# Optimization experiments

Measured on AMD Instinct MI355X. Metric: run time of the kernel, lower is better.

Reference implementation:

```python
import jax, jax.numpy as jnp
import numpy as np

H, W = 48, 48
L = H * W            # 2304 tokens
D = 256              # d_model
NH = 8               # heads (self and memory attn)
FF = 1024            # dim_feedforward
T = 2                # memory frames
BS = 1
GN_GROUPS = 32       # GNActDWConv2d default groups


def layernorm(x, g, b, eps=1e-5):
    m = jnp.mean(x, -1, keepdims=True)
    v = jnp.mean((x - m) ** 2, -1, keepdims=True)
    return (x - m) * jax.lax.rsqrt(v + eps) * g + b


def linear(x, Wt, b):
    # torch nn.Linear convention: Wt is [out, in]
    return x @ Wt.T + b


def mha_core(Q, K, V, nhead):
    # Q [Lq, bs, C], K/V [Lk, bs, C]; AOT MultiheadAttention core (eval: no dropout)
    Lq, bs, C = Q.shape
    hd = C // nhead
    Qh = (Q / np.float32(np.sqrt(hd))).reshape(Lq, bs, nhead, hd).transpose(1, 2, 0, 3)
    Kh = K.reshape(-1, bs, nhead, hd).transpose(1, 2, 0, 3)
    Vh = V.reshape(-1, bs, nhead, hd).transpose(1, 2, 0, 3)
    attn = jax.nn.softmax(jnp.einsum('bhqd,bhkd->bhqk', Qh, Kh), axis=-1)
    out = jnp.einsum('bhqk,bhkd->bhqd', attn, Vh)
    return out.transpose(2, 0, 1, 3).reshape(Lq, bs, C)


def groupnorm(x, g, b, groups, eps=1e-5):
    bs, c, h, w = x.shape
    xg = x.reshape(bs, groups, c // groups, h, w)
    m = jnp.mean(xg, (2, 3, 4), keepdims=True)
    v = jnp.mean((xg - m) ** 2, (2, 3, 4), keepdims=True)
    xg = (xg - m) * jax.lax.rsqrt(v + eps)
    return xg.reshape(bs, c, h, w) * g[None, :, None, None] + b[None, :, None, None]


def dwconv5(x, k):
    # depthwise 5x5, padding=2; x [bs,c,h,w], k [c,1,5,5]
    return jax.lax.conv_general_dilated(x, k, (1, 1), ((2, 2), (2, 2)),
                                        feature_group_count=x.shape[1])


def setup_inputs() -> dict:
    key = jax.random.key(0)
    ks = jax.random.split(key, 16)
    rn = lambda i, shape, s=1.0: jax.random.normal(ks[i], shape, jnp.float32) * s
    w = 0.02
    inp = {
        'tgt': rn(0, (L, BS, D)),
        'global_K': rn(1, (T, L, BS, D)),
        'global_V': rn(2, (T, L, BS, D)),
        'local_K': rn(3, (L, BS, D)),
        'local_V': rn(4, (L, BS, D)),
        # LayerNorms
        'ln1_g': jnp.ones(D, jnp.float32), 'ln1_b': jnp.zeros(D, jnp.float32),
        'ln2_g': jnp.ones(D, jnp.float32), 'ln2_b': jnp.zeros(D, jnp.float32),
        'ln3_g': jnp.ones(D, jnp.float32), 'ln3_b': jnp.zeros(D, jnp.float32),
        'ln4_g': jnp.ones(D, jnp.float32), 'ln4_b': jnp.zeros(D, jnp.float32),
        # self_attn (use_linear=True) Q/K/V + projection
        'sa_Wq': rn(5, (D, D), w), 'sa_bq': jnp.zeros(D, jnp.float32),
        'sa_Wk': rn(6, (D, D), w), 'sa_bk': jnp.zeros(D, jnp.float32),
        'sa_Wv': rn(7, (D, D), w), 'sa_bv': jnp.zeros(D, jnp.float32),
        'sa_Wo': rn(8, (D, D), w), 'sa_bo': jnp.zeros(D, jnp.float32),
        # block linear_Q
        'Wq': rn(9, (D, D), w), 'bq': jnp.zeros(D, jnp.float32),
        # long/short term attn projections (use_linear=False)
        'lt_Wo': rn(10, (D, D), w), 'lt_bo': jnp.zeros(D, jnp.float32),
        'st_Wo': rn(11, (D, D), w), 'st_bo': jnp.zeros(D, jnp.float32),
        # FFN: linear1 -> GN+GELU+DWConv -> linear2
        'W1': rn(12, (FF, D), w), 'b1': jnp.zeros(FF, jnp.float32),
        'gn_g': jnp.ones(FF, jnp.float32), 'gn_b': jnp.zeros(FF, jnp.float32),
        'dw_k': rn(13, (FF, 1, 5, 5), 0.05),
        'W2': rn(14, (D, FF), w), 'b2': jnp.zeros(D, jnp.float32),
    }
    return inp


def reference(tgt, global_K, global_V, local_K, local_V,
              ln1_g, ln1_b, ln2_g, ln2_b, ln3_g, ln3_b, ln4_g, ln4_b,
              sa_Wq, sa_bq, sa_Wk, sa_bk, sa_Wv, sa_bv, sa_Wo, sa_bo,
              Wq, bq, lt_Wo, lt_bo, st_Wo, st_bo,
              W1, b1, gn_g, gn_b, dw_k, W2, b2):
    # --- stage 1: self-attention ---
    _tgt = layernorm(tgt, ln1_g, ln1_b)
    q = linear(_tgt, sa_Wq, sa_bq)
    k = linear(_tgt, sa_Wk, sa_bk)
    v = linear(_tgt, sa_Wv, sa_bv)
    tgt2 = linear(mha_core(q, k, v, NH), sa_Wo, sa_bo)
    tgt = tgt + tgt2  # droppath is identity at eval

    # --- stage 2: long-term + short-term memory cross-attention ---
    _tgt = layernorm(tgt, ln2_g, ln2_b)
    curr_Q = linear(_tgt, Wq, bq)
    curr_K = curr_Q
    curr_V = _tgt

    flat_K = global_K.reshape(-1, BS, D)  # [T*L, bs, D]
    flat_V = global_V.reshape(-1, BS, D)
    tgt2 = linear(mha_core(curr_Q, flat_K, flat_V, NH), lt_Wo, lt_bo)

    k_st = layernorm(local_K + curr_K, ln4_g, ln4_b)
    v_st = layernorm(local_V + curr_V, ln4_g, ln4_b)
    tgt3 = linear(mha_core(curr_Q, k_st, v_st, NH), st_Wo, st_bo)

    tgt = tgt + tgt2 + tgt3

    # --- stage 3: FFN with GN + GELU + depthwise conv ---
    _tgt = layernorm(tgt, ln3_g, ln3_b)
    x = linear(_tgt, W1, b1)                        # [L, bs, FF]
    x = x.reshape(H, W, BS, FF).transpose(2, 3, 0, 1)  # [bs, FF, H, W]
    x = jax.nn.gelu(groupnorm(x, gn_g, gn_b, GN_GROUPS), approximate=False)
    x = dwconv5(x, dw_k)
    x = x.reshape(BS, FF, L).transpose(2, 0, 1)     # [L, bs, FF]
    tgt2 = linear(x, W2, b2)
    return tgt + tgt2
```

## Files before the change

kernel.cpp:

```cpp
#include <hip/hip_runtime.h>
#include <hip/hip_bf16.h>

#define L   2304
#define D   256
#define NHD 8
#define HD  32
#define FF  1024
#define HH  48
#define WWW 48
#define SPL 4
#define RCH 24
#define RP  (L / RCH)
#define S2LOG 0.25503486f

typedef unsigned short bfraw;
typedef __attribute__((ext_vector_type(8))) short s8v;
typedef __attribute__((ext_vector_type(4))) float f4v;

__device__ __forceinline__ bfraw f2b(float x) {
    __hip_bfloat16 h = __float2bfloat16(x);
    return __builtin_bit_cast(bfraw, h);
}

__global__ __launch_bounds__(256) void diag_kernel(float* __restrict__ out, float c, int n)
{
    int i = blockIdx.x * 256 + threadIdx.x;
    if (i < n) out[i] = c;
}

__global__ __launch_bounds__(256) void ln_kernel(
    const float* __restrict__ inA, const float* __restrict__ inB,
    const float* __restrict__ g, const float* __restrict__ b,
    float* __restrict__ out, bfraw* __restrict__ outb)
{
    int row = blockIdx.x, t = threadIdx.x;
    size_t idx = (size_t)row * D + t;
    float v = inA[idx];
    if (inB) v += inB[idx];
    __shared__ float rs[256], rq[256];
    rs[t] = v; rq[t] = v * v;
    __syncthreads();
    for (int o = 128; o > 0; o >>= 1) {
        if (t < o) { rs[t] += rs[t + o]; rq[t] += rq[t + o]; }
        __syncthreads();
    }
    float mean = rs[0] * (1.f / D);
    float var  = rq[0] * (1.f / D) - mean * mean;
    float rstd = rsqrtf(var + 1e-5f);
    float r = (v - mean) * rstd * g[t] + b[t];
    if (out)  out[idx]  = r;
    if (outb) outb[idx] = f2b(r);
}

__global__ __launch_bounds__(256) void ln2cvt(
    const float* __restrict__ t5, const float* __restrict__ lV,
    const float* __restrict__ g2, const float* __restrict__ b2,
    const float* __restrict__ g4, const float* __restrict__ b4,
    bfraw* __restrict__ out2b, float* __restrict__ outv,
    const float* __restrict__ gK, bfraw* __restrict__ kb1,
    const float* __restrict__ gV, bfraw* __restrict__ vtb1)
{
    __shared__ float rs[256], rq[256];
    __shared__ float Ls[32][33];
    int t = threadIdx.x;
    if (blockIdx.x < L) {
        int row = blockIdx.x;
        size_t idx = (size_t)row * D + t;
        float v = t5[idx];
        rs[t] = v; rq[t] = v * v;
        __syncthreads();
        for (int o = 128; o > 0; o >>= 1) {
            if (t < o) { rs[t] += rs[t + o]; rq[t] += rq[t + o]; }
            __syncthreads();
        }
        float mean = rs[0] * (1.f / D);
        float var  = rq[0] * (1.f / D) - mean * mean;
        float rstd = rsqrtf(var + 1e-5f);
        float r2 = (v - mean) * rstd * g2[t] + b2[t];
        out2b[idx] = f2b(r2);
        float u = r2 + lV[idx];
        __syncthreads();
        rs[t] = u; rq[t] = u * u;
        __syncthreads();
        for (int o = 128; o > 0; o >>= 1) {
            if (t < o) { rs[t] += rs[t + o]; rq[t] += rq[t + o]; }
            __syncthreads();
        }
        float mean2 = rs[0] * (1.f / D);
        float var2  = rq[0] * (1.f / D) - mean2 * mean2;
        float rstd2 = rsqrtf(var2 + 1e-5f);
        outv[idx] = (u - mean2) * rstd2 * g4[t] + b4[t];
    } else {
        int idx = blockIdx.x - L;
        int ix = idx % (2 * L / 32), iy = idx / (2 * L / 32);
        if (iy < NHD) {
            int h = iy, n0 = ix * 32;
            const int N = 2 * L;
            int nl = t >> 3, dq = t & 7;
            float4 v = *reinterpret_cast<const float4*>(gV + (size_t)(n0 + nl) * D + h * HD + dq * 4);
            Ls[nl][dq*4+0] = v.x; Ls[nl][dq*4+1] = v.y;
            Ls[nl][dq*4+2] = v.z; Ls[nl][dq*4+3] = v.w;
            __syncthreads();
            int dl = t >> 3, nq = t & 7;
            ushort4 o;
            o.x = f2b(Ls[nq*4+0][dl]); o.y = f2b(Ls[nq*4+1][dl]);
            o.z = f2b(Ls[nq*4+2][dl]); o.w = f2b(Ls[nq*4+3][dl]);
            *reinterpret_cast<ushort4*>(vtb1 + (size_t)(h * HD + dl) * N + n0 + nq * 4) = o;
        } else {
            size_t i = ((size_t)(ix * 8 + (iy - NHD)) * 256 + t) * 4;
            float4 v = *reinterpret_cast<const float4*>(gK + i);
            ushort4 o;
            o.x = f2b(v.x); o.y = f2b(v.y); o.z = f2b(v.z); o.w = f2b(v.w);
            *reinterpret_cast<ushort4*>(kb1 + i) = o;
        }
    }
}

__global__ __launch_bounds__(256) void ln_cvtT(
    const float* __restrict__ t1, const float* __restrict__ lK,
    const float* __restrict__ g4, const float* __restrict__ b4,
    bfraw* __restrict__ kb2,
    const float* __restrict__ vsrc, bfraw* __restrict__ vtb2)
{
    __shared__ float rs[256], rq[256];
    __shared__ float Ls[32][33];
    int t = threadIdx.x;
    if (blockIdx.x < L) {
        int row = blockIdx.x;
        size_t idx = (size_t)row * D + t;
        float v = t1[idx] + lK[idx];
        rs[t] = v; rq[t] = v * v;
        __syncthreads();
        for (int o = 128; o > 0; o >>= 1) {
            if (t < o) { rs[t] += rs[t + o]; rq[t] += rq[t + o]; }
            __syncthreads();
        }
        float mean = rs[0] * (1.f / D);
        float var  = rq[0] * (1.f / D) - mean * mean;
        float rstd = rsqrtf(var + 1e-5f);
        kb2[idx] = f2b((v - mean) * rstd * g4[t] + b4[t]);
    } else {
        int idx = blockIdx.x - L;
        int n0 = (idx >> 3) * 32, h = idx & 7;
        int nl = t >> 3, dq = t & 7;
        float4 v = *reinterpret_cast<const float4*>(vsrc + (size_t)(n0 + nl) * D + h * HD + dq * 4);
        Ls[nl][dq*4+0] = v.x; Ls[nl][dq*4+1] = v.y;
        Ls[nl][dq*4+2] = v.z; Ls[nl][dq*4+3] = v.w;
        __syncthreads();
        int dl = t >> 3, nq = t & 7;
        ushort4 o;
        o.x = f2b(Ls[nq*4+0][dl]); o.y = f2b(Ls[nq*4+1][dl]);
        o.z = f2b(Ls[nq*4+2][dl]); o.w = f2b(Ls[nq*4+3][dl]);
        *reinterpret_cast<ushort4*>(vtb2 + (size_t)(h * HD + dl) * L + n0 + nq * 4) = o;
    }
}

__global__ __launch_bounds__(256) void gemm_mfma(
    const bfraw* __restrict__ A, const float* __restrict__ W,
    const float* __restrict__ bias, const float* res, float* out,
    bfraw* __restrict__ outb, float oscale,
    int M, int N, int K)
{
    __shared__ __attribute__((aligned(16))) short Wl[64][32];
    int t = threadIdx.x;
    int w = t >> 6, l = t & 63;
    int lo = l & 15, quad = l >> 4;
    int m0 = blockIdx.x * 32, n0 = blockIdx.y * 64;
    int wr = (w & 1) * 16, wc = (w >> 1) * 32;
    f4v acc[2];
    acc[0] = (f4v){0.f, 0.f, 0.f, 0.f};
    acc[1] = (f4v){0.f, 0.f, 0.f, 0.f};

    int aswz = (quad ^ ((lo >> 2) & 3)) * 8;
    int srow = t >> 3, spart = t & 7;
    const bfraw* ap = A + (size_t)(m0 + wr + lo) * K + quad * 8;

    for (int k0 = 0; k0 < K; k0 += 32) {
        float4 w4[2];
        #pragma unroll
        for (int i = 0; i < 2; i++)
            w4[i] = *reinterpret_cast<const float4*>(W + (size_t)(n0 + i * 32 + srow) * K + k0 + spart * 4);
        s8v af = *reinterpret_cast<const s8v*>(ap + k0);
        __syncthreads();
        #pragma unroll
        for (int i = 0; i < 2; i++) {
            int row = i * 32 + srow;
            int col = ((spart >> 1) ^ ((row >> 2) & 3)) * 8 + (spart & 1) * 4;
            ushort4 wb;
            wb.x = f2b(w4[i].x); wb.y = f2b(w4[i].y); wb.z = f2b(w4[i].z); wb.w = f2b(w4[i].w);
            *reinterpret_cast<ushort4*>(&Wl[row][col]) = wb;
        }
        __syncthreads();
        #pragma unroll
        for (int j = 0; j < 2; j++) {
            int rw = wc + j * 16 + lo;
            s8v wf = *reinterpret_cast<const s8v*>(&Wl[rw][aswz]);
            acc[j] = __builtin_amdgcn_mfma_f32_16x16x32_bf16(af, wf, acc[j], 0, 0, 0);
        }
    }

    #pragma unroll
    for (int j = 0; j < 2; j++) {
        #pragma unroll
        for (int r = 0; r < 4; r++) {
            int mrow = m0 + wr + quad * 4 + r;
            int ncol = n0 + wc + j * 16 + lo;
            float v = acc[j][r] + bias[ncol];
            size_t idx = (size_t)mrow * N + ncol;
            if (res) v += res[idx];
            if (out) out[idx] = v;
            if (outb) outb[idx] = f2b(v * oscale);
        }
    }
}

__global__ __launch_bounds__(256) void gemm_dual(
    const bfraw* __restrict__ A1, const float* __restrict__ W1, const float* __restrict__ b1,
    const bfraw* __restrict__ A2, const float* __restrict__ W2, const float* __restrict__ b2,
    const float* __restrict__ res, float* __restrict__ out)
{
    __shared__ __attribute__((aligned(16))) short Wl[64][32];
    int t = threadIdx.x;
    int w = t >> 6, l = t & 63;
    int lo = l & 15, quad = l >> 4;
    int m0 = blockIdx.x * 32, n0 = blockIdx.y * 64;
    int wr = (w & 1) * 16, wc = (w >> 1) * 32;
    f4v acc[2];
    acc[0] = (f4v){0.f, 0.f, 0.f, 0.f};
    acc[1] = (f4v){0.f, 0.f, 0.f, 0.f};

    int aswz = (quad ^ ((lo >> 2) & 3)) * 8;
    int srow = t >> 3, spart = t & 7;

    #pragma unroll
    for (int half = 0; half < 2; half++) {
        const bfraw* ap = (half ? A2 : A1) + (size_t)(m0 + wr + lo) * D + quad * 8;
        const float* W  = half ? W2 : W1;
        for (int k0 = 0; k0 < D; k0 += 32) {
            float4 w4[2];
            #pragma unroll
            for (int i = 0; i < 2; i++)
                w4[i] = *reinterpret_cast<const float4*>(W + (size_t)(n0 + i * 32 + srow) * D + k0 + spart * 4);
            s8v af = *reinterpret_cast<const s8v*>(ap + k0);
            __syncthreads();
            #pragma unroll
            for (int i = 0; i < 2; i++) {
                int row = i * 32 + srow;
                int col = ((spart >> 1) ^ ((row >> 2) & 3)) * 8 + (spart & 1) * 4;
                ushort4 wb;
                wb.x = f2b(w4[i].x); wb.y = f2b(w4[i].y); wb.z = f2b(w4[i].z); wb.w = f2b(w4[i].w);
                *reinterpret_cast<ushort4*>(&Wl[row][col]) = wb;
            }
            __syncthreads();
            #pragma unroll
            for (int j = 0; j < 2; j++) {
                int rw = wc + j * 16 + lo;
                s8v wf = *reinterpret_cast<const s8v*>(&Wl[rw][aswz]);
                acc[j] = __builtin_amdgcn_mfma_f32_16x16x32_bf16(af, wf, acc[j], 0, 0, 0);
            }
        }
    }

    #pragma unroll
    for (int j = 0; j < 2; j++) {
        #pragma unroll
        for (int r = 0; r < 4; r++) {
            int mrow = m0 + wr + quad * 4 + r;
            int ncol = n0 + wc + j * 16 + lo;
            size_t idx = (size_t)mrow * D + ncol;
            out[idx] = acc[j][r] + b1[ncol] + b2[ncol] + res[idx];
        }
    }
}

__global__ __launch_bounds__(256) void gemm_qkv(
    const bfraw* __restrict__ A,
    const float* __restrict__ Wq_, const float* __restrict__ bq_,
    const float* __restrict__ Wk_, const float* __restrict__ bk_,
    const float* __restrict__ Wv_, const float* __restrict__ bv_,
    bfraw* __restrict__ qb, bfraw* __restrict__ kb, bfraw* __restrict__ vtb)
{
    __shared__ __attribute__((aligned(16))) short Wl[64][32];
    int t = threadIdx.x;
    int w = t >> 6, l = t & 63;
    int lo = l & 15, quad = l >> 4;
    int sel = blockIdx.y >> 2;
    int m0 = blockIdx.x * 32, n0 = (blockIdx.y & 3) * 64;
    int wr = (w & 1) * 16, wc = (w >> 1) * 32;
    const float* W    = (sel == 0) ? Wq_ : (sel == 1) ? Wk_ : Wv_;
    const float* bias = (sel == 0) ? bq_ : (sel == 1) ? bk_ : bv_;
    f4v acc[2];
    acc[0] = (f4v){0.f, 0.f, 0.f, 0.f};
    acc[1] = (f4v){0.f, 0.f, 0.f, 0.f};

    int aswz = (quad ^ ((lo >> 2) & 3)) * 8;
    int srow = t >> 3, spart = t & 7;
    const bfraw* ap = A + (size_t)(m0 + wr + lo) * D + quad * 8;

    for (int k0 = 0; k0 < D; k0 += 32) {
        float4 w4[2];
        #pragma unroll
        for (int i = 0; i < 2; i++)
            w4[i] = *reinterpret_cast<const float4*>(W + (size_t)(n0 + i * 32 + srow) * D + k0 + spart * 4);
        s8v af = *reinterpret_cast<const s8v*>(ap + k0);
        __syncthreads();
        #pragma unroll
        for (int i = 0; i < 2; i++) {
            int row = i * 32 + srow;
            int col = ((spart >> 1) ^ ((row >> 2) & 3)) * 8 + (spart & 1) * 4;
            ushort4 wb;
            wb.x = f2b(w4[i].x); wb.y = f2b(w4[i].y); wb.z = f2b(w4[i].z); wb.w = f2b(w4[i].w);
            *reinterpret_cast<ushort4*>(&Wl[row][col]) = wb;
        }
        __syncthreads();
        #pragma unroll
        for (int j = 0; j < 2; j++) {
            int rw = wc + j * 16 + lo;
            s8v wf = *reinterpret_cast<const s8v*>(&Wl[rw][aswz]);
            acc[j] = __builtin_amdgcn_mfma_f32_16x16x32_bf16(af, wf, acc[j], 0, 0, 0);
        }
    }

    #pragma unroll
    for (int j = 0; j < 2; j++) {
        #pragma unroll
        for (int r = 0; r < 4; r++) {
            int mrow = m0 + wr + quad * 4 + r;
            int ncol = n0 + wc + j * 16 + lo;
            float v = acc[j][r] + bias[ncol];
            if (sel == 0)      qb[(size_t)mrow * D + ncol] = f2b(v * S2LOG);
            else if (sel == 1) kb[(size_t)mrow * D + ncol] = f2b(v);
            else               vtb[(size_t)ncol * L + mrow] = f2b(v);
        }
    }
}

__device__ __forceinline__ void attn_core(
    const bfraw* __restrict__ Qb, const bfraw* __restrict__ Kb,
    const bfraw* __restrict__ Vt, float* __restrict__ OP,
    float* __restrict__ ML, int Lk, int chunk, int zz,
    short (*Ks)[32], short (*Vts)[72], short (*Ps)[72], float (*Tb)[33])
{
    int t = threadIdx.x;
    int w = t >> 6, l = t & 63;
    int h = blockIdx.y, q0 = blockIdx.x * 64 + w * 16;
    int lo = l & 15, quad = l >> 4;
    int kb = zz * chunk, ke = kb + chunk;

    s8v qf = *reinterpret_cast<const s8v*>(Qb + (size_t)(q0 + lo) * D + h * HD + quad * 8);
    int kswz = (quad ^ ((lo >> 2) & 3)) * 8;

    int skey = t >> 2, spart = t & 3;
    int kcol = (spart ^ ((skey >> 2) & 3)) * 8;
    int sd = t >> 3, svp = t & 7;
    const bfraw* kp = Kb + (size_t)skey * D + h * HD + spart * 8;
    const bfraw* vp = Vt + (size_t)(h * HD + sd) * Lk + svp * 8;

    float l_r = 0.f;
    f4v o0 = {0.f, 0.f, 0.f, 0.f}, o1 = {0.f, 0.f, 0.f, 0.f};

    for (int k0 = kb; k0 < ke; k0 += 64) {
        s8v kv = *reinterpret_cast<const s8v*>(kp + (size_t)k0 * D);
        s8v vv = *reinterpret_cast<const s8v*>(vp + k0);
        __syncthreads();
        *reinterpret_cast<s8v*>(&Ks[skey][kcol]) = kv;
        *reinterpret_cast<s8v*>(&Vts[sd][svp * 8]) = vv;
        __syncthreads();

        f4v sc4[4];
        #pragma unroll
        for (int s = 0; s < 4; s++) {
            s8v kf = *reinterpret_cast<const s8v*>(&Ks[lo + 16 * s][kswz]);
            sc4[s] = __builtin_amdgcn_mfma_f32_16x16x32_bf16(kf, qf, (f4v){0.f,0.f,0.f,0.f}, 0, 0, 0);
        }
        float ls = 0.f;
        #pragma unroll
        for (int s = 0; s < 4; s++) {
            float p0 = __builtin_amdgcn_exp2f(sc4[s][0]);
            float p1 = __builtin_amdgcn_exp2f(sc4[s][1]);
            float p2 = __builtin_amdgcn_exp2f(sc4[s][2]);
            float p3 = __builtin_amdgcn_exp2f(sc4[s][3]);
            ls += p0 + p1 + p2 + p3;
            ushort4 pk;
            pk.x = f2b(p0); pk.y = f2b(p1); pk.z = f2b(p2); pk.w = f2b(p3);
            *reinterpret_cast<ushort4*>(&Ps[lo][s * 16 + quad * 4]) = pk;
        }
        ls += __shfl_xor(ls, 16);
        ls += __shfl_xor(ls, 32);
        l_r += ls;
        #pragma unroll
        for (int kc = 0; kc < 2; kc++) {
            s8v pf = *reinterpret_cast<const s8v*>(&Ps[lo][kc * 32 + quad * 8]);
            s8v v0 = *reinterpret_cast<const s8v*>(&Vts[lo][kc * 32 + quad * 8]);
            s8v v1 = *reinterpret_cast<const s8v*>(&Vts[16 + lo][kc * 32 + quad * 8]);
            o0 = __builtin_amdgcn_mfma_f32_16x16x32_bf16(v0, pf, o0, 0, 0, 0);
            o1 = __builtin_amdgcn_mfma_f32_16x16x32_bf16(v1, pf, o1, 0, 0, 0);
        }
    }

    #pragma unroll
    for (int r = 0; r < 4; r++) {
        Tb[lo][quad * 4 + r]      = o0[r];
        Tb[lo][16 + quad * 4 + r] = o1[r];
    }
    float* Oz = OP + (size_t)zz * L * D;
    int ql = l >> 2, dq = (l & 3) * 8;
    float4 u0, u1;
    u0.x = Tb[ql][dq + 0]; u0.y = Tb[ql][dq + 1];
    u0.z = Tb[ql][dq + 2]; u0.w = Tb[ql][dq + 3];
    u1.x = Tb[ql][dq + 4]; u1.y = Tb[ql][dq + 5];
    u1.z = Tb[ql][dq + 6]; u1.w = Tb[ql][dq + 7];
    *reinterpret_cast<float4*>(Oz + (size_t)(q0 + ql) * D + h * HD + dq)     = u0;
    *reinterpret_cast<float4*>(Oz + (size_t)(q0 + ql) * D + h * HD + dq + 4) = u1;
    if (l < 16)
        ML[((size_t)zz * NHD + h) * L + q0 + lo] = l_r;
}

__global__ __launch_bounds__(256) void attn_mfma_split(
    const bfraw* __restrict__ Qb, const bfraw* __restrict__ Kb,
    const bfraw* __restrict__ Vt, float* __restrict__ OP,
    float* __restrict__ ML, int Lk, int chunk)
{
    __shared__ __attribute__((aligned(16))) short Ks[64][32];
    __shared__ __attribute__((aligned(16))) short Vts[32][72];
    __shared__ __attribute__((aligned(16))) short Ps[4][16][72];
    __shared__ float Tb[4][16][33];
    int w = threadIdx.x >> 6;
    attn_core(Qb, Kb, Vt, OP, ML, Lk, chunk, blockIdx.z, Ks, Vts, Ps[w], Tb[w]);
}

__global__ __launch_bounds__(256) void attn_ltst(
    const bfraw* __restrict__ Qb,
    const bfraw* __restrict__ K_lt, const bfraw* __restrict__ V_lt,
    float* __restrict__ OP_lt, float* __restrict__ ML_lt,
    const bfraw* __restrict__ K_st, const bfraw* __restrict__ V_st,
    float* __restrict__ OP_st, float* __restrict__ ML_st)
{
    __shared__ __attribute__((aligned(16))) short Ks[64][32];
    __shared__ __attribute__((aligned(16))) short Vts[32][72];
    __shared__ __attribute__((aligned(16))) short Ps[4][16][72];
    __shared__ float Tb[4][16][33];
    int w = threadIdx.x >> 6;
    int z = blockIdx.z;
    if (z < 2)
        attn_core(Qb, K_lt, V_lt, OP_lt, ML_lt, 2 * L, L, z, Ks, Vts, Ps[w], Tb[w]);
    else
        attn_core(Qb, K_st, V_st, OP_st, ML_st, L, L / 2, z - 2, Ks, Vts, Ps[w], Tb[w]);
}

__global__ __launch_bounds__(256) void attn_combine(
    const float* __restrict__ OP, const float* __restrict__ ML,
    bfraw* __restrict__ Ob)
{
    int q = blockIdx.x, t = threadIdx.x, h = t >> 5;
    float wl = 0.f, acc = 0.f;
    #pragma unroll
    for (int s = 0; s < SPL; s++) {
        wl  += ML[((size_t)s * NHD + h) * L + q];
        acc += OP[(size_t)s * L * D + (size_t)q * D + t];
    }
    Ob[(size_t)q * D + t] = f2b(acc / wl);
}

__global__ __launch_bounds__(256) void combine2_both(
    const float* __restrict__ OP_lt, const float* __restrict__ ML_lt, bfraw* __restrict__ Ob_lt,
    const float* __restrict__ OP_st, const float* __restrict__ ML_st, bfraw* __restrict__ Ob_st)
{
    int q = blockIdx.x, t = threadIdx.x, h = t >> 5;
    const float* OP = blockIdx.y ? OP_st : OP_lt;
    const float* ML = blockIdx.y ? ML_st : ML_lt;
    bfraw* Ob = blockIdx.y ? Ob_st : Ob_lt;
    float wl = 0.f, acc = 0.f;
    #pragma unroll
    for (int s = 0; s < 2; s++) {
        wl  += ML[((size_t)s * NHD + h) * L + q];
        acc += OP[(size_t)s * L * D + (size_t)q * D + t];
    }
    Ob[(size_t)q * D + t] = f2b(acc / wl);
}

__global__ __launch_bounds__(256) void gn_stats_part(
    const float* __restrict__ X, float* __restrict__ ps)
{
    int g = blockIdx.x, rc = blockIdx.y, t = threadIdx.x;
    int cq = (t & 7) * 4;
    int rl = t >> 3;
    int r0 = rc * RP;
    float s = 0.f, sq = 0.f;
    #pragma unroll
    for (int p = 0; p < RP / 32; p++) {
        int l = r0 + p * 32 + rl;
        float4 v = *reinterpret_cast<const float4*>(X + (size_t)l * FF + g * 32 + cq);
        s  += v.x + v.y + v.z + v.w;
        sq += v.x*v.x + v.y*v.y + v.z*v.z + v.w*v.w;
    }
    __shared__ float rs[256], rq[256];
    rs[t] = s; rq[t] = sq;
    __syncthreads();
    for (int o = 128; o > 0; o >>= 1) {
        if (t < o) { rs[t] += rs[t + o]; rq[t] += rq[t + o]; }
        __syncthreads();
    }
    if (t == 0) {
        ps[(g * RCH + rc) * 2]     = rs[0];
        ps[(g * RCH + rc) * 2 + 1] = rq[0];
    }
}

__global__ __launch_bounds__(256) void gn_gelu_dwconv(
    const float* __restrict__ X, const float* __restrict__ ps,
    const float* __restrict__ gg, const float* __restrict__ gb,
    const float* __restrict__ Kw, bfraw* __restrict__ Y)
{
    __shared__ float tile[144][64];
    int h0 = blockIdx.x * 8, w0 = blockIdx.y * 8, c0 = blockIdx.z * 64;
    int t = threadIdx.x;
    int c = t & 63;
    int cg = (c0 + c) >> 5;
    float s = 0.f, sq = 0.f;
    #pragma unroll
    for (int i = 0; i < RCH; i++) {
        s  += ps[(cg * RCH + i) * 2];
        sq += ps[(cg * RCH + i) * 2 + 1];
    }
    float n = (float)(L * 32);
    float mu = s / n;
    float rs = rsqrtf(sq / n - mu * mu + 1e-5f);
    float ga = gg[c0 + c], be = gb[c0 + c];

    for (int i = t; i < 144 * 64; i += 256) {
        int sp = i >> 6;
        int hy = h0 + (sp / 12) - 2, wx = w0 + (sp % 12) - 2;
        float v = 0.f;
        if (hy >= 0 && hy < HH && wx >= 0 && wx < WWW) {
            float x = X[(size_t)(hy * WWW + wx) * FF + c0 + c];
            x = (x - mu) * rs * ga + be;
            v = 0.5f * x * (1.f + erff(x * 0.70710678118654752f));
        }
        tile[sp][c] = v;
    }
    float kw[25];
    #pragma unroll
    for (int i = 0; i < 25; i++) kw[i] = Kw[(size_t)(c0 + c) * 25 + i];
    __syncthreads();

    int sgrp = t >> 6;
    for (int sIdx = 0; sIdx < 16; sIdx++) {
        int sp = sgrp * 16 + sIdx;
        int oh = sp >> 3, ow = sp & 7;
        float acc = 0.f;
        #pragma unroll
        for (int ky = 0; ky < 5; ky++)
            #pragma unroll
            for (int kx = 0; kx < 5; kx++)
                acc += tile[(oh + ky) * 12 + ow + kx][c] * kw[ky * 5 + kx];
        Y[(size_t)((h0 + oh) * WWW + w0 + ow) * FF + c0 + c] = f2b(acc);
    }
}

extern "C" void kernel_launch(void* const* d_in, const int* in_sizes, int n_in,
                              void* d_out, int out_size, void* d_ws, size_t ws_size,
                              hipStream_t stream)
{
    (void)in_sizes;
    float* out = (float*)d_out;

    if (n_in != 34) {
        diag_kernel<<<(out_size + 255) / 256, 256, 0, stream>>>(out, 2000.f, out_size);
        return;
    }

    const float* tgt    = (const float*)d_in[0];
    const float* gK     = (const float*)d_in[1];
    const float* gV     = (const float*)d_in[2];
    const float* lK     = (const float*)d_in[3];
    const float* lV     = (const float*)d_in[4];
    const float* ln1_g  = (const float*)d_in[5];
    const float* ln1_b  = (const float*)d_in[6];
    const float* ln2_g  = (const float*)d_in[7];
    const float* ln2_b  = (const float*)d_in[8];
    const float* ln3_g  = (const float*)d_in[9];
    const float* ln3_b  = (const float*)d_in[10];
    const float* ln4_g  = (const float*)d_in[11];
    const float* ln4_b  = (const float*)d_in[12];
    const float* sa_Wq  = (const float*)d_in[13];
    const float* sa_bq  = (const float*)d_in[14];
    const float* sa_Wk  = (const float*)d_in[15];
    const float* sa_bk  = (const float*)d_in[16];
    const float* sa_Wv  = (const float*)d_in[17];
    const float* sa_bv  = (const float*)d_in[18];
    const float* sa_Wo  = (const float*)d_in[19];
    const float* sa_bo  = (const float*)d_in[20];
    const float* Wq     = (const float*)d_in[21];
    const float* bq     = (const float*)d_in[22];
    const float* lt_Wo  = (const float*)d_in[23];
    const float* lt_bo  = (const float*)d_in[24];
    const float* st_Wo  = (const float*)d_in[25];
    const float* st_bo  = (const float*)d_in[26];
    const float* W1w    = (const float*)d_in[27];
    const float* b1w    = (const float*)d_in[28];
    const float* gn_g   = (const float*)d_in[29];
    const float* gn_b   = (const float*)d_in[30];
    const float* dw_k   = (const float*)d_in[31];
    const float* W2w    = (const float*)d_in[32];
    const float* b2w    = (const float*)d_in[33];

    const size_t LD = (size_t)L * D;
    const size_t NEED = (6 * LD + (size_t)L * FF + 64) * 4;
    float* ws = (float*)d_ws;
    float* t0 = ws + 0 * LD;
    float* t1 = ws + 1 * LD;
    float* t2 = ws + 2 * LD;
    float* t3 = ws + 3 * LD;
    float* t4 = ws + 4 * LD;
    float* t5 = ws + 5 * LD;
    float* X1 = t0;
    float* X2 = ws + 6 * LD;
    bfraw* qb   = (bfraw*)X2;
    bfraw* kb1  = qb + LD;
    bfraw* vtb1 = qb + 3 * LD;
    bfraw* kb2  = qb + 5 * LD;
    bfraw* vtb2 = qb + 6 * LD;
    float* OP   = ws;
    float* OPlt = t0;
    float* OPst = t2;
    float* ML   = X2 + (7 * LD) / 2;
    float* MLlt = ML;
    float* MLst = ML + 2 * (size_t)NHD * L;
    float* PS   = ML;
    bfraw* t0b  = (bfraw*)t0;
    bfraw* t3b  = (bfraw*)t3;
    bfraw* t4b  = (bfraw*)t4;
    bfraw* obLT = t4b;
    bfraw* obST = t4b + LD;
    bfraw* X2b  = (bfraw*)X2;

    if (ws_size < NEED) {
        int wsMiB = (int)(ws_size >> 20); if (wsMiB > 63) wsMiB = 63;
        diag_kernel<<<(out_size + 255) / 256, 256, 0, stream>>>(out, 64.f + (float)wsMiB, out_size);
        return;
    }

    dim3 gDD(L / 32, D / 64);
    dim3 gDF(L / 32, FF / 64);
    dim3 gQKV(L / 32, 12);
    dim3 gATS(L / 64, NHD, SPL);
    dim3 gAT2(L / 64, NHD, 4);
    dim3 gC2(L, 2);
    dim3 gGN(32, RCH);
    dim3 gDW(6, 6, 16);

    ln_kernel<<<L, 256, 0, stream>>>(tgt, nullptr, ln1_g, ln1_b, nullptr, t0b);
    gemm_qkv<<<gQKV, 256, 0, stream>>>(t0b, sa_Wq, sa_bq, sa_Wk, sa_bk, sa_Wv, sa_bv,
                                       qb, kb2, vtb2);
    attn_mfma_split<<<gATS, 256, 0, stream>>>(qb, kb2, vtb2, OP, ML, L, L / SPL);
    attn_combine<<<L, 256, 0, stream>>>(OP, ML, t4b);
    gemm_mfma<<<gDD, 256, 0, stream>>>(t4b, sa_Wo, sa_bo, tgt, t5, nullptr, 1.f, L, D, D);

    ln2cvt<<<L + (2 * L / 32) * (NHD + 8), 256, 0, stream>>>(
        t5, lV, ln2_g, ln2_b, ln4_g, ln4_b, t3b, t0, gK, kb1, gV, vtb1);
    gemm_mfma<<<gDD, 256, 0, stream>>>(t3b, Wq, bq, nullptr, t1, qb, S2LOG, L, D, D);
    ln_cvtT<<<L + (L / 32) * NHD, 256, 0, stream>>>(t1, lK, ln4_g, ln4_b, kb2, t0, vtb2);
    attn_ltst<<<gAT2, 256, 0, stream>>>(qb, kb1, vtb1, OPlt, MLlt, kb2, vtb2, OPst, MLst);
    combine2_both<<<gC2, 256, 0, stream>>>(OPlt, MLlt, obLT, OPst, MLst, obST);
    gemm_dual<<<gDD, 256, 0, stream>>>(obLT, lt_Wo, lt_bo, obST, st_Wo, st_bo, t5, t5);

    ln_kernel<<<L, 256, 0, stream>>>(t5, nullptr, ln3_g, ln3_b, nullptr, t4b);
    gemm_mfma<<<gDF, 256, 0, stream>>>(t4b, W1w, b1w, nullptr, X1, nullptr, 1.f, L, FF, D);
    gn_stats_part<<<gGN, 256, 0, stream>>>(X1, PS);
    gn_gelu_dwconv<<<gDW, 256, 0, stream>>>(X1, PS, gn_g, gn_b, dw_k, X2b);
    gemm_mfma<<<gDD, 256, 0, stream>>>(X2b, W2w, b2w, t5, out, nullptr, 1.f, L, D, FF);
}
```

Baseline: 311.0 us.

## Fuse split-attention combine into attention kernels via last-block atomic counters

Removes the separate attn_combine and combine2_both launches. Each attention block now increments a per-(query tile, head) atomic counter after writing its partials, and the last block to finish performs the normalization and bf16 write-out. The counters are zeroed inside the first layernorm launch. This saves two kernel launches and a pass over the partials, at the cost of threadfences, atomics and a serialized tail on the last-arriving blocks.

After: 650.8 us. +109.3%, slower.

```diff
diff --git a/kernel.cpp b/kernel.cpp
--- a/kernel.cpp
+++ b/kernel.cpp
@@ -31,9 +31,13 @@
 __global__ __launch_bounds__(256) void ln_kernel(
     const float* __restrict__ inA, const float* __restrict__ inB,
     const float* __restrict__ g, const float* __restrict__ b,
-    float* __restrict__ out, bfraw* __restrict__ outb)
+    float* __restrict__ out, bfraw* __restrict__ outb,
+    int* __restrict__ zcnt)
 {
     int row = blockIdx.x, t = threadIdx.x;
+    if (zcnt && row == 0) {
+        zcnt[t] = 0; zcnt[t + 256] = 0; zcnt[t + 512] = 0; zcnt[t + 768] = 0;
+    }
     size_t idx = (size_t)row * D + t;
     float v = inA[idx];
     if (inB) v += inB[idx];
@@ -416,17 +420,54 @@
         ML[((size_t)zz * NHD + h) * L + q0 + lo] = l_r;
 }
 
+__device__ __forceinline__ void combine_tail(
+    const float* __restrict__ OP, const float* __restrict__ ML,
+    bfraw* __restrict__ Ob, int spl, int bx, int h)
+{
+    int t = threadIdx.x;
+    int row = bx * 64 + (t >> 2);
+    int col = h * HD + (t & 3) * 8;
+    float wl = 0.f;
+    float a[8] = {0.f, 0.f, 0.f, 0.f, 0.f, 0.f, 0.f, 0.f};
+    for (int s = 0; s < spl; s++) {
+        wl += ML[((size_t)s * NHD + h) * L + row];
+        const float* p = OP + (size_t)s * L * D + (size_t)row * D + col;
+        float4 x = *reinterpret_cast<const float4*>(p);
+        float4 y = *reinterpret_cast<const float4*>(p + 4);
+        a[0] += x.x; a[1] += x.y; a[2] += x.z; a[3] += x.w;
+        a[4] += y.x; a[5] += y.y; a[6] += y.z; a[7] += y.w;
+    }
+    float inv = 1.f / wl;
+    ushort4 o0, o1;
+    o0.x = f2b(a[0]*inv); o0.y = f2b(a[1]*inv); o0.z = f2b(a[2]*inv); o0.w = f2b(a[3]*inv);
+    o1.x = f2b(a[4]*inv); o1.y = f2b(a[5]*inv); o1.z = f2b(a[6]*inv); o1.w = f2b(a[7]*inv);
+    *reinterpret_cast<ushort4*>(Ob + (size_t)row * D + col)     = o0;
+    *reinterpret_cast<ushort4*>(Ob + (size_t)row * D + col + 4) = o1;
+}
+
 __global__ __launch_bounds__(256) void attn_mfma_split(
     const bfraw* __restrict__ Qb, const bfraw* __restrict__ Kb,
     const bfraw* __restrict__ Vt, float* __restrict__ OP,
-    float* __restrict__ ML, int Lk, int chunk)
+    float* __restrict__ ML, int Lk, int chunk,
+    int* __restrict__ cnt, bfraw* __restrict__ Ob)
 {
     __shared__ __attribute__((aligned(16))) short Ks[64][32];
     __shared__ __attribute__((aligned(16))) short Vts[32][72];
     __shared__ __attribute__((aligned(16))) short Ps[4][16][72];
     __shared__ float Tb[4][16][33];
+    __shared__ int lastFlag;
     int w = threadIdx.x >> 6;
     attn_core(Qb, Kb, Vt, OP, ML, Lk, chunk, blockIdx.z, Ks, Vts, Ps[w], Tb[w]);
+    __threadfence();
+    if (threadIdx.x == 0) {
+        int old = atomicAdd(&cnt[blockIdx.x * NHD + blockIdx.y], 1);
+        lastFlag = (old == SPL - 1);
+    }
+    __syncthreads();
+    if (lastFlag) {
+        __threadfence();
+        combine_tail(OP, ML, Ob, SPL, blockIdx.x, blockIdx.y);
+    }
 }
 
 __global__ __launch_bounds__(256) void attn_ltst(
@@ -434,49 +475,33 @@
     const bfraw* __restrict__ K_lt, const bfraw* __restrict__ V_lt,
     float* __restrict__ OP_lt, float* __restrict__ ML_lt,
     const bfraw* __restrict__ K_st, const bfraw* __restrict__ V_st,
-    float* __restrict__ OP_st, float* __restrict__ ML_st)
+    float* __restrict__ OP_st, float* __restrict__ ML_st,
+    int* __restrict__ cnt, bfraw* __restrict__ Ob_lt, bfraw* __restrict__ Ob_st)
 {
     __shared__ __attribute__((aligned(16))) short Ks[64][32];
     __shared__ __attribute__((aligned(16))) short Vts[32][72];
     __shared__ __attribute__((aligned(16))) short Ps[4][16][72];
     __shared__ float Tb[4][16][33];
+    __shared__ int lastFlag;
     int w = threadIdx.x >> 6;
     int z = blockIdx.z;
-    if (z < 2)
+    bool isLT = (z < 2);
+    if (isLT)
         attn_core(Qb, K_lt, V_lt, OP_lt, ML_lt, 2 * L, L, z, Ks, Vts, Ps[w], Tb[w]);
     else
         attn_core(Qb, K_st, V_st, OP_st, ML_st, L, L / 2, z - 2, Ks, Vts, Ps[w], Tb[w]);
-}
-
-__global__ __launch_bounds__(256) void attn_combine(
-    const float* __restrict__ OP, const float* __restrict__ ML,
-    bfraw* __restrict__ Ob)
-{
-    int q = blockIdx.x, t = threadIdx.x, h = t >> 5;
-    float wl = 0.f, acc = 0.f;
-    #pragma unroll
-    for (int s = 0; s < SPL; s++) {
-        wl  += ML[((size_t)s * NHD + h) * L + q];
-        acc += OP[(size_t)s * L * D + (size_t)q * D + t];
-    }
-    Ob[(size_t)q * D + t] = f2b(acc / wl);
-}
-
-__global__ __launch_bounds__(256) void combine2_both(
-    const float* __restrict__ OP_lt, const float* __restrict__ ML_lt, bfraw* __restrict__ Ob_lt,
-    const float* __restrict__ OP_st, const float* __restrict__ ML_st, bfraw* __restrict__ Ob_st)
-{
-    int q = blockIdx.x, t = threadIdx.x, h = t >> 5;
-    const float* OP = blockIdx.y ? OP_st : OP_lt;
-    const float* ML = blockIdx.y ? ML_st : ML_lt;
-    bfraw* Ob = blockIdx.y ? Ob_st : Ob_lt;
-    float wl = 0.f, acc = 0.f;
-    #pragma unroll
-    for (int s = 0; s < 2; s++) {
-        wl  += ML[((size_t)s * NHD + h) * L + q];
-        acc += OP[(size_t)s * L * D + (size_t)q * D + t];
-    }
-    Ob[(size_t)q * D + t] = f2b(acc / wl);
+    __threadfence();
+    if (threadIdx.x == 0) {
+        int idx = (isLT ? 0 : 288) + blockIdx.x * NHD + blockIdx.y;
+        int old = atomicAdd(&cnt[idx], 1);
+        lastFlag = (old == 1);
+    }
+    __syncthreads();
+    if (lastFlag) {
+        __threadfence();
+        if (isLT) combine_tail(OP_lt, ML_lt, Ob_lt, 2, blockIdx.x, blockIdx.y);
+        else      combine_tail(OP_st, ML_st, Ob_st, 2, blockIdx.x, blockIdx.y);
+    }
 }
 
 __global__ __launch_bounds__(256) void gn_stats_part(
@@ -628,6 +653,7 @@
     float* MLlt = ML;
     float* MLst = ML + 2 * (size_t)NHD * L;
     float* PS   = ML;
+    int*   CNT  = (int*)(ML + 75000);
     bfraw* t0b  = (bfraw*)t0;
     bfraw* t3b  = (bfraw*)t3;
     bfraw* t4b  = (bfraw*)t4;
@@ -646,26 +672,24 @@
     dim3 gQKV(L / 32, 12);
     dim3 gATS(L / 64, NHD, SPL);
     dim3 gAT2(L / 64, NHD, 4);
-    dim3 gC2(L, 2);
     dim3 gGN(32, RCH);
     dim3 gDW(6, 6, 16);
 
-    ln_kernel<<<L, 256, 0, stream>>>(tgt, nullptr, ln1_g, ln1_b, nullptr, t0b);
+    ln_kernel<<<L, 256, 0, stream>>>(tgt, nullptr, ln1_g, ln1_b, nullptr, t0b, CNT);
     gemm_qkv<<<gQKV, 256, 0, stream>>>(t0b, sa_Wq, sa_bq, sa_Wk, sa_bk, sa_Wv, sa_bv,
                                        qb, kb2, vtb2);
-    attn_mfma_split<<<gATS, 256, 0, stream>>>(qb, kb2, vtb2, OP, ML, L, L / SPL);
-    attn_combine<<<L, 256, 0, stream>>>(OP, ML, t4b);
+    attn_mfma_split<<<gATS, 256, 0, stream>>>(qb, kb2, vtb2, OP, ML, L, L / SPL, CNT, t4b);
     gemm_mfma<<<gDD, 256, 0, stream>>>(t4b, sa_Wo, sa_bo, tgt, t5, nullptr, 1.f, L, D, D);
 
     ln2cvt<<<L + (2 * L / 32) * (NHD + 8), 256, 0, stream>>>(
         t5, lV, ln2_g, ln2_b, ln4_g, ln4_b, t3b, t0, gK, kb1, gV, vtb1);
     gemm_mfma<<<gDD, 256, 0, stream>>>(t3b, Wq, bq, nullptr, t1, qb, S2LOG, L, D, D);
     ln_cvtT<<<L + (L / 32) * NHD, 256, 0, stream>>>(t1, lK, ln4_g, ln4_b, kb2, t0, vtb2);
-    attn_ltst<<<gAT2, 256, 0, stream>>>(qb, kb1, vtb1, OPlt, MLlt, kb2, vtb2, OPst, MLst);
-    combine2_both<<<gC2, 256, 0, stream>>>(OPlt, MLlt, obLT, OPst, MLst, obST);
+    attn_ltst<<<gAT2, 256, 0, stream>>>(qb, kb1, vtb1, OPlt, MLlt, kb2, vtb2, OPst, MLst,
+                                        CNT + 288, obLT, obST);
     gemm_dual<<<gDD, 256, 0, stream>>>(obLT, lt_Wo, lt_bo, obST, st_Wo, st_bo, t5, t5);
 
-    ln_kernel<<<L, 256, 0, stream>>>(t5, nullptr, ln3_g, ln3_b, nullptr, t4b);
+    ln_kernel<<<L, 256, 0, stream>>>(t5, nullptr, ln3_g, ln3_b, nullptr, t4b, nullptr);
     gemm_mfma<<<gDF, 256, 0, stream>>>(t4b, W1w, b1w, nullptr, X1, nullptr, 1.f, L, FF, D);
     gn_stats_part<<<gGN, 256, 0, stream>>>(X1, PS);
     gn_gelu_dwconv<<<gDW, 256, 0, stream>>>(X1, PS, gn_g, gn_b, dw_k, X2b);
```
